# Performance work log

Measured on AMD Instinct MI355X. Metric: run time of the kernel, lower is better.

The kernel has to match this reference:

```python
import jax, jax.numpy as jnp
import numpy as np

N = 100_000   # nodes
E = 1_600_000 # edges (avg degree 16)
IN, HID, MID, OUT = 128, 64, 128, 32


def setup_inputs() -> dict:
    key = jax.random.key(0)
    ks = jax.random.split(key, 8)
    def glorot(k, fan_in, fan_out):
        s = (6.0 / (fan_in + fan_out)) ** 0.5
        return jax.random.uniform(k, (fan_in, fan_out), jnp.float32, -s, s)
    x = jax.random.normal(ks[0], (N, IN), jnp.float32)
    edge_index = jax.random.randint(ks[1], (2, E), 0, N, jnp.int64)
    return {
        "x": x,
        "edge_index": edge_index,
        "W1": glorot(ks[2], IN, HID),  "b1": jnp.zeros((HID,), jnp.float32),
        "Wl1": glorot(ks[3], HID, MID), "bl1": jnp.zeros((MID,), jnp.float32),
        "Wl2": glorot(ks[4], MID, HID), "bl2": jnp.zeros((HID,), jnp.float32),
        "W2": glorot(ks[5], HID, OUT), "b2": jnp.zeros((OUT,), jnp.float32),
    }


def _gcn_conv(h, W, b, src, dst, norm, n_nodes):
    # PyG GCNConv: linear transform, normalized gather-scatter aggregation, bias
    m = (h @ W)[src] * norm[:, None]                       # [E+N, out_dim]
    out = jax.ops.segment_sum(m, dst, num_segments=n_nodes)
    return out + b


def reference(x, edge_index, W1, b1, Wl1, bl1, Wl2, bl2, W2, b2):
    n = x.shape[0]
    loops = jnp.arange(n, dtype=edge_index.dtype)
    src = jnp.concatenate([edge_index[0], loops])          # add self-loops
    dst = jnp.concatenate([edge_index[1], loops])
    # symmetric normalization D^-1/2 A D^-1/2 with unit edge weights
    deg = jax.ops.segment_sum(jnp.ones_like(src, jnp.float32), dst, num_segments=n)
    dis = jnp.where(deg > 0, jax.lax.rsqrt(jnp.maximum(deg, 1.0)), 0.0)
    norm = dis[src] * dis[dst]                             # [E+N]
    # dropout layers are identity in eval mode
    h = jax.nn.relu(_gcn_conv(x, W1, b1, src, dst, norm, n))
    h = jax.nn.relu(jax.nn.relu(h @ Wl1 + bl1) @ Wl2 + bl2)
    return _gcn_conv(h, W2, b2, src, dst, norm, n)
```

## Files before the change

### kernel.cpp

```cpp
#include <hip/hip_runtime.h>


static constexpr int TPB = 256;

__global__ __launch_bounds__(TPB) void k_cnt_init(int* __restrict__ cnt, int n) {
  int i = blockIdx.x * TPB + threadIdx.x;
  if (i < n) cnt[i] = 0;
}

__global__ __launch_bounds__(TPB) void k_cnt(const int* __restrict__ dst,
                                             int* __restrict__ cnt, int e) {
  int i = blockIdx.x * TPB + threadIdx.x;
  if (i < e) atomicAdd(&cnt[dst[i]], 1);
}

__global__ __launch_bounds__(TPB) void k_dis(const int* __restrict__ cnt,
                                             float* __restrict__ dis, int n) {
  int i = blockIdx.x * TPB + threadIdx.x;
  if (i < n) dis[i] = rsqrtf((float)(cnt[i] + 1));
}

__global__ __launch_bounds__(TPB) void k_scanA(const int* __restrict__ cnt,
                                               int* __restrict__ bsums, int n) {
  int base = blockIdx.x * 1024 + threadIdx.x * 4;
  int s = 0;
#pragma unroll
  for (int q = 0; q < 4; ++q) if (base + q < n) s += cnt[base + q];
  int lane = threadIdx.x & 63, wv = threadIdx.x >> 6;
#pragma unroll
  for (int off = 32; off; off >>= 1) s += __shfl_down(s, off);
  __shared__ int ls[4];
  if (lane == 0) ls[wv] = s;
  __syncthreads();
  if (threadIdx.x == 0) bsums[blockIdx.x] = ls[0] + ls[1] + ls[2] + ls[3];
}

__global__ void k_scanB(int* __restrict__ bsums, int nb,
                        int* __restrict__ rowstart, int n) {
  int acc = 0;
  for (int i = 0; i < nb; ++i) { int v = bsums[i]; bsums[i] = acc; acc += v; }
  rowstart[n] = acc;
}

__global__ __launch_bounds__(TPB) void k_scanC(const int* __restrict__ cnt,
                                               const int* __restrict__ bsums,
                                               int* __restrict__ rowstart,
                                               int* __restrict__ cursor, int n) {
  int base = blockIdx.x * 1024 + threadIdx.x * 4;
  int v[4] = {0, 0, 0, 0};
#pragma unroll
  for (int q = 0; q < 4; ++q) if (base + q < n) v[q] = cnt[base + q];
  int mysum = v[0] + v[1] + v[2] + v[3];
  int s = mysum;
  int lane = threadIdx.x & 63, wv = threadIdx.x >> 6;
#pragma unroll
  for (int off = 1; off < 64; off <<= 1) {
    int t = __shfl_up(s, off);
    if (lane >= off) s += t;
  }
  __shared__ int ls[4];
  if (lane == 63) ls[wv] = s;
  __syncthreads();
  int woff = 0;
  for (int w2 = 0; w2 < wv; ++w2) woff += ls[w2];
  int ex = bsums[blockIdx.x] + woff + (s - mysum);
#pragma unroll
  for (int q = 0; q < 4; ++q) {
    if (base + q < n) { rowstart[base + q] = ex; cursor[base + q] = 0; }
    ex += v[q];
  }
}

__global__ __launch_bounds__(TPB) void k_fill(const int* __restrict__ src,
                                              const int* __restrict__ dst,
                                              const int* __restrict__ rowstart,
                                              int* __restrict__ cursor,
                                              int* __restrict__ csr, int e) {
  int i = blockIdx.x * TPB + threadIdx.x;
  if (i >= e) return;
  int d = dst[i];
  int pos = rowstart[d] + atomicAdd(&cursor[d], 1);
  csr[pos] = src[i];
}

__global__ __launch_bounds__(TPB) void k_lin1(
    const float* __restrict__ x, const float* __restrict__ W1,
    const float* __restrict__ dis, float* __restrict__ hs1, int n) {
  const int node = blockIdx.x * TPB + threadIdx.x;
  const int nc = node < n ? node : n - 1;

  float acc[64];
#pragma unroll
  for (int j = 0; j < 64; ++j) acc[j] = 0.f;

  float4 xv = *(const float4*)&x[(size_t)nc * 128];
#pragma unroll 1
  for (int kk = 0; kk < 32; ++kk) {
    float4 xn = *(const float4*)&x[(size_t)nc * 128 + (((kk + 1) & 31) * 4)];
#pragma unroll
    for (int q = 0; q < 4; ++q) {
      const float xs = q == 0 ? xv.x : q == 1 ? xv.y : q == 2 ? xv.z : xv.w;
      const int k = kk * 4 + q;
#pragma unroll
      for (int j = 0; j < 64; ++j)
        acc[j] = fmaf(xs, W1[k * 64 + j], acc[j]);
    }
    xv = xn;
  }

  if (node < n) {
    const float d = dis[nc];
#pragma unroll
    for (int jj = 0; jj < 16; ++jj) {
      float4 o;
      o.x = acc[jj * 4 + 0] * d;
      o.y = acc[jj * 4 + 1] * d;
      o.z = acc[jj * 4 + 2] * d;
      o.w = acc[jj * 4 + 3] * d;
      *(float4*)&hs1[(size_t)node * 64 + jj * 4] = o;
    }
  }
}

__global__ __launch_bounds__(TPB) void k_agg1(
    const int* __restrict__ rowstart, const int* __restrict__ csr,
    const float* __restrict__ hs1, const float* __restrict__ dis,
    const float* __restrict__ b1, float* __restrict__ agg1, int n) {
  int node = (blockIdx.x * TPB + threadIdx.x) >> 6;
  int lane = threadIdx.x & 63;
  if (node >= n) return;
  const int g = lane >> 4, sub = lane & 15;
  const int beg = rowstart[node], end = rowstart[node + 1];
  float4 acc = {0.f, 0.f, 0.f, 0.f};
  for (int p = beg + g; p < end; p += 4) {
    int s = csr[p];
    float4 v = *(const float4*)&hs1[(size_t)s * 64 + sub * 4];
    acc.x += v.x; acc.y += v.y; acc.z += v.z; acc.w += v.w;
  }
#pragma unroll
  for (int m = 16; m <= 32; m <<= 1) {
    acc.x += __shfl_xor(acc.x, m);
    acc.y += __shfl_xor(acc.y, m);
    acc.z += __shfl_xor(acc.z, m);
    acc.w += __shfl_xor(acc.w, m);
  }
  if (lane < 16) {
    float4 self = *(const float4*)&hs1[(size_t)node * 64 + sub * 4];
    float4 bb = *(const float4*)&b1[sub * 4];
    float d = dis[node];
    float4 o;
    o.x = fmaf(acc.x + self.x, d, bb.x);
    o.y = fmaf(acc.y + self.y, d, bb.y);
    o.z = fmaf(acc.z + self.z, d, bb.z);
    o.w = fmaf(acc.w + self.w, d, bb.w);
    *(float4*)&agg1[(size_t)node * 64 + sub * 4] = o;
  }
}

__global__ __launch_bounds__(64) void k_mlp(
    const float* __restrict__ agg1,
    const float* __restrict__ Wl1, const float* __restrict__ bl1,
    const float* __restrict__ Wl2, const float* __restrict__ bl2,
    const float* __restrict__ W2, const float* __restrict__ dis,
    float* __restrict__ ms2, int n) {
  __shared__ float tT[64 * 64];
  const int lane = threadIdx.x;
  const int node = blockIdx.x * 64 + lane;
  const int nc = node < n ? node : n - 1;

  float t1[128];
#pragma unroll
  for (int j = 0; j < 128; ++j) t1[j] = bl1[j];

  float h = fmaxf(agg1[(size_t)nc * 64 + 0], 0.f);
#pragma unroll 1
  for (int k = 0; k < 64; ++k) {
    float hn = fmaxf(agg1[(size_t)nc * 64 + ((k + 1) & 63)], 0.f);
#pragma unroll
    for (int j = 0; j < 128; ++j)
      t1[j] = fmaf(h, Wl1[k * 128 + j], t1[j]);
    h = hn;
  }

  float t2[64];
#pragma unroll
  for (int m = 0; m < 64; ++m) t2[m] = bl2[m];

#pragma unroll 1
  for (int c = 0; c < 2; ++c) {
#pragma unroll
    for (int j2 = 0; j2 < 64; ++j2) tT[j2 * 64 + lane] = fmaxf(t1[c * 64 + j2], 0.f);
    __syncthreads();
#pragma unroll 1
    for (int j2 = 0; j2 < 64; ++j2) {
      float tj = tT[j2 * 64 + lane];
      const int j = c * 64 + j2;
#pragma unroll
      for (int m = 0; m < 64; ++m)
        t2[m] = fmaf(tj, Wl2[j * 64 + m], t2[m]);
    }
    __syncthreads();
  }

#pragma unroll
  for (int m = 0; m < 64; ++m) tT[m * 64 + lane] = fmaxf(t2[m], 0.f);
  __syncthreads();

  float mo[32];
#pragma unroll
  for (int o = 0; o < 32; ++o) mo[o] = 0.f;
#pragma unroll 1
  for (int m = 0; m < 64; ++m) {
    float tm = tT[m * 64 + lane];
#pragma unroll
    for (int o = 0; o < 32; ++o)
      mo[o] = fmaf(tm, W2[m * 32 + o], mo[o]);
  }

  if (node < n) {
    const float d = dis[nc];
#pragma unroll
    for (int oo = 0; oo < 8; ++oo) {
      float4 v;
      v.x = mo[oo * 4 + 0] * d;
      v.y = mo[oo * 4 + 1] * d;
      v.z = mo[oo * 4 + 2] * d;
      v.w = mo[oo * 4 + 3] * d;
      *(float4*)&ms2[(size_t)node * 32 + oo * 4] = v;
    }
  }
}

__global__ __launch_bounds__(TPB) void k_agg2(
    const int* __restrict__ rowstart, const int* __restrict__ csr,
    const float* __restrict__ ms2, const float* __restrict__ dis,
    const float* __restrict__ b2, float* __restrict__ out, int n) {
  int node = (blockIdx.x * TPB + threadIdx.x) >> 6;
  int lane = threadIdx.x & 63;
  if (node >= n) return;
  const int g = lane >> 3, sub = lane & 7;
  const int beg = rowstart[node], end = rowstart[node + 1];
  float4 acc = {0.f, 0.f, 0.f, 0.f};
  for (int p = beg + g; p < end; p += 8) {
    int s = csr[p];
    float4 v = *(const float4*)&ms2[(size_t)s * 32 + sub * 4];
    acc.x += v.x; acc.y += v.y; acc.z += v.z; acc.w += v.w;
  }
#pragma unroll
  for (int m = 8; m <= 32; m <<= 1) {
    acc.x += __shfl_xor(acc.x, m);
    acc.y += __shfl_xor(acc.y, m);
    acc.z += __shfl_xor(acc.z, m);
    acc.w += __shfl_xor(acc.w, m);
  }
  if (lane < 8) {
    float4 self = *(const float4*)&ms2[(size_t)node * 32 + sub * 4];
    float4 bb = *(const float4*)&b2[sub * 4];
    float d = dis[node];
    float4 o;
    o.x = fmaf(acc.x + self.x, d, bb.x);
    o.y = fmaf(acc.y + self.y, d, bb.y);
    o.z = fmaf(acc.z + self.z, d, bb.z);
    o.w = fmaf(acc.w + self.w, d, bb.w);
    *(float4*)&out[(size_t)node * 32 + sub * 4] = o;
  }
}

extern "C" void kernel_launch(void* const* d_in, const int* in_sizes, int n_in,
                              void* d_out, int out_size, void* d_ws, size_t ws_size,
                              hipStream_t stream) {
  const float* x   = (const float*)d_in[0];
  const int* ei    = (const int*)d_in[1];
  const float* W1  = (const float*)d_in[2];
  const float* b1  = (const float*)d_in[3];
  const float* Wl1 = (const float*)d_in[4];
  const float* bl1 = (const float*)d_in[5];
  const float* Wl2 = (const float*)d_in[6];
  const float* bl2 = (const float*)d_in[7];
  const float* W2  = (const float*)d_in[8];
  const float* b2  = (const float*)d_in[9];
  float* out = (float*)d_out;

  const int n = in_sizes[0] / 128;
  const int e = in_sizes[1] / 2;
  const int* src = ei;
  const int* dst = ei + e;

  int* wsw = (int*)d_ws;
  float* dis     = (float*)wsw;
  int* cnt       = wsw + n;
  int* rowstart  = wsw + 2 * n;
  int* cursor    = wsw + 3 * n + 4;
  int* bsums     = wsw + 4 * n + 4;
  int* csr       = wsw + 4 * n + 1028;
  float* hs1     = (float*)(wsw + 4 * n + 1028 + e);
  float* ms2     = hs1;
  float* agg1    = hs1 + 64 * (size_t)n;

  const int gN = (n + TPB - 1) / TPB;
  const int gE = (e + TPB - 1) / TPB;
  const int nb = (n + 1023) / 1024;
  const int nwave = (n + 63) / 64;
  const int gAgg = (int)(((long long)n * 64 + TPB - 1) / TPB);

  k_cnt_init<<<gN, TPB, 0, stream>>>(cnt, n);
  k_cnt<<<gE, TPB, 0, stream>>>(dst, cnt, e);
  k_dis<<<gN, TPB, 0, stream>>>(cnt, dis, n);
  k_scanA<<<nb, TPB, 0, stream>>>(cnt, bsums, n);
  k_scanB<<<1, 1, 0, stream>>>(bsums, nb, rowstart, n);
  k_scanC<<<nb, TPB, 0, stream>>>(cnt, bsums, rowstart, cursor, n);
  k_fill<<<gE, TPB, 0, stream>>>(src, dst, rowstart, cursor, csr, e);
  k_lin1<<<(n + TPB - 1) / TPB, TPB, 0, stream>>>(x, W1, dis, hs1, n);
  k_agg1<<<gAgg, TPB, 0, stream>>>(rowstart, csr, hs1, dis, b1, agg1, n);
  k_mlp<<<nwave, 64, 0, stream>>>(agg1, Wl1, bl1, Wl2, bl2, W2, dis, ms2, n);
  k_agg2<<<gAgg, TPB, 0, stream>>>(rowstart, csr, ms2, dis, b2, out, n);
}
```

Baseline: 623.2 us.

## Fuse MLP layers per hidden unit, drop shared-memory staging in k_mlp

Restructures the per-node MLP so each of the 128 hidden units is computed as a dot product over a register-resident input row and immediately consumed by the second layer. This removes the 128-element t1 register array, the LDS transpose buffer and its barriers. A small kernel pre-transposes Wl1 so the dot-product reads run over contiguous memory. The intent is lower register pressure and better occupancy, at the cost of an extra launch and workspace slots for the transposed weights.

```diff
diff --git a/kernel.cpp b/kernel.cpp
--- a/kernel.cpp
+++ b/kernel.cpp
@@ -81,6 +81,15 @@
   int d = dst[i];
   int pos = rowstart[d] + atomicAdd(&cursor[d], 1);
   csr[pos] = src[i];
+}
+
+__global__ __launch_bounds__(TPB) void k_wt(const float* __restrict__ Wl1,
+                                            float* __restrict__ Wl1T) {
+  int i = blockIdx.x * TPB + threadIdx.x;
+  if (i < 128 * 64) {
+    int j = i >> 6, k = i & 63;
+    Wl1T[i] = Wl1[k * 128 + j];
+  }
 }
 
 __global__ __launch_bounds__(TPB) void k_lin1(
@@ -159,59 +168,46 @@
 
 __global__ __launch_bounds__(64) void k_mlp(
     const float* __restrict__ agg1,
-    const float* __restrict__ Wl1, const float* __restrict__ bl1,
+    const float* __restrict__ Wl1T, const float* __restrict__ bl1,
     const float* __restrict__ Wl2, const float* __restrict__ bl2,
     const float* __restrict__ W2, const float* __restrict__ dis,
     float* __restrict__ ms2, int n) {
-  __shared__ float tT[64 * 64];
   const int lane = threadIdx.x;
   const int node = blockIdx.x * 64 + lane;
   const int nc = node < n ? node : n - 1;
 
-  float t1[128];
-#pragma unroll
-  for (int j = 0; j < 128; ++j) t1[j] = bl1[j];
-
-  float h = fmaxf(agg1[(size_t)nc * 64 + 0], 0.f);
-#pragma unroll 1
-  for (int k = 0; k < 64; ++k) {
-    float hn = fmaxf(agg1[(size_t)nc * 64 + ((k + 1) & 63)], 0.f);
-#pragma unroll
-    for (int j = 0; j < 128; ++j)
-      t1[j] = fmaf(h, Wl1[k * 128 + j], t1[j]);
-    h = hn;
+  float h[64];
+#pragma unroll
+  for (int i = 0; i < 16; ++i) {
+    float4 v = *(const float4*)&agg1[(size_t)nc * 64 + i * 4];
+    h[i * 4 + 0] = fmaxf(v.x, 0.f);
+    h[i * 4 + 1] = fmaxf(v.y, 0.f);
+    h[i * 4 + 2] = fmaxf(v.z, 0.f);
+    h[i * 4 + 3] = fmaxf(v.w, 0.f);
   }
 
   float t2[64];
 #pragma unroll
   for (int m = 0; m < 64; ++m) t2[m] = bl2[m];
 
-#pragma unroll 1
-  for (int c = 0; c < 2; ++c) {
-#pragma unroll
-    for (int j2 = 0; j2 < 64; ++j2) tT[j2 * 64 + lane] = fmaxf(t1[c * 64 + j2], 0.f);
-    __syncthreads();
-#pragma unroll 1
-    for (int j2 = 0; j2 < 64; ++j2) {
-      float tj = tT[j2 * 64 + lane];
-      const int j = c * 64 + j2;
-#pragma unroll
-      for (int m = 0; m < 64; ++m)
-        t2[m] = fmaf(tj, Wl2[j * 64 + m], t2[m]);
-    }
-    __syncthreads();
-  }
-
-#pragma unroll
-  for (int m = 0; m < 64; ++m) tT[m * 64 + lane] = fmaxf(t2[m], 0.f);
-  __syncthreads();
+#pragma unroll 2
+  for (int j = 0; j < 128; ++j) {
+    float t = bl1[j];
+#pragma unroll
+    for (int k = 0; k < 64; ++k)
+      t = fmaf(h[k], Wl1T[j * 64 + k], t);
+    t = fmaxf(t, 0.f);
+#pragma unroll
+    for (int m = 0; m < 64; ++m)
+      t2[m] = fmaf(t, Wl2[j * 64 + m], t2[m]);
+  }
 
   float mo[32];
 #pragma unroll
   for (int o = 0; o < 32; ++o) mo[o] = 0.f;
-#pragma unroll 1
+#pragma unroll 2
   for (int m = 0; m < 64; ++m) {
-    float tm = tT[m * 64 + lane];
+    float tm = fmaxf(t2[m], 0.f);
 #pragma unroll
     for (int o = 0; o < 32; ++o)
       mo[o] = fmaf(tm, W2[m * 32 + o], mo[o]);
@@ -292,8 +288,9 @@
   int* rowstart  = wsw + 2 * n;
   int* cursor    = wsw + 3 * n + 4;
   int* bsums     = wsw + 4 * n + 4;
-  int* csr       = wsw + 4 * n + 1028;
-  float* hs1     = (float*)(wsw + 4 * n + 1028 + e);
+  float* wl1t    = (float*)(wsw + 4 * n + 1028);
+  int* csr       = wsw + 4 * n + 1028 + 8192;
+  float* hs1     = (float*)(wsw + 4 * n + 1028 + 8192 + e);
   float* ms2     = hs1;
   float* agg1    = hs1 + 64 * (size_t)n;
 
@@ -310,8 +307,9 @@
   k_scanB<<<1, 1, 0, stream>>>(bsums, nb, rowstart, n);
   k_scanC<<<nb, TPB, 0, stream>>>(cnt, bsums, rowstart, cursor, n);
   k_fill<<<gE, TPB, 0, stream>>>(src, dst, rowstart, cursor, csr, e);
+  k_wt<<<32, TPB, 0, stream>>>(Wl1, wl1t);
   k_lin1<<<(n + TPB - 1) / TPB, TPB, 0, stream>>>(x, W1, dis, hs1, n);
   k_agg1<<<gAgg, TPB, 0, stream>>>(rowstart, csr, hs1, dis, b1, agg1, n);
-  k_mlp<<<nwave, 64, 0, stream>>>(agg1, Wl1, bl1, Wl2, bl2, W2, dis, ms2, n);
+  k_mlp<<<nwave, 64, 0, stream>>>(agg1, wl1t, bl1, Wl2, bl2, W2, dis, ms2, n);
   k_agg2<<<gAgg, TPB, 0, stream>>>(rowstart, csr, ms2, dis, b2, out, n);
 }
```

After: 606.9 us. 1.03x faster.
